# Kernel tuning notes

Measured on AMD Instinct MI355X. Metric: run time of the kernel, lower is better.

## Reference

```python
import jax, jax.numpy as jnp
import numpy as np

N_MEL = 80
NEG = -1e30  # log-zero sentinel, as in the torch module


def setup_inputs() -> dict:
    key = jax.random.key(0)
    k1, k2, k3, k4 = jax.random.split(key, 4)
    B, txt_T, mel_T = 16, 128, 512
    mu_logvar = jax.random.normal(k1, (B, txt_T, 2 * N_MEL), dtype=jnp.float32)
    melspec = jax.random.normal(k2, (B, N_MEL, mel_T), dtype=jnp.float32)
    text_lengths = jax.random.randint(k3, (B,), txt_T // 2, txt_T + 1, dtype=jnp.int32)
    mel_lengths = jax.random.randint(k4, (B,), mel_T // 2, mel_T + 1, dtype=jnp.int32)
    return dict(mu_logvar=mu_logvar, melspec=melspec,
                text_lengths=text_lengths, mel_lengths=mel_lengths)


def _log_prob_matrix(mu_logvar, melspec):
    # mu_logvar: [B, txt_T, 2*n_mel]; melspec: [B, n_mel, mel_T]
    mu = mu_logvar[:, :, :N_MEL]            # [B, txt_T, n_mel]
    logvar = mu_logvar[:, :, N_MEL:]        # [B, txt_T, n_mel]
    x = jnp.transpose(melspec, (0, 2, 1))   # [B, mel_T, n_mel]
    diff = x[:, None, :, :] - mu[:, :, None, :]          # [B, txt_T, mel_T, n_mel]
    quad = diff * diff * jnp.exp(-logvar)[:, :, None, :] + logvar[:, :, None, :]
    return -0.5 * jnp.mean(quad, axis=3)    # [B, txt_T, mel_T]


def _log_alpha_last(log_prob_matrix, text_lengths, mel_lengths):
    B, txt_T, mel_T = log_prob_matrix.shape
    # init: log_alpha[:, :, 0] = NEG except [:,0,0] = logp[:,0,0]
    init = jnp.full((B, txt_T), NEG, log_prob_matrix.dtype).at[:, 0].set(log_prob_matrix[:, 0, 0])
    logp_t = jnp.moveaxis(log_prob_matrix, 2, 0)  # [mel_T, B, txt_T]

    def step(prev, lp):
        # shift-by-one along text axis (monotonic alignment: stay or advance)
        shifted = jnp.concatenate([jnp.full((B, 1), NEG, prev.dtype), prev[:, :-1]], axis=1)
        cur = jnp.logaddexp(prev + 1e-30, shifted + 1e-30) + lp
        return cur, cur

    _, rest = jax.lax.scan(step, init, logp_t[1:])
    log_alpha = jnp.concatenate([init[None], rest], axis=0)  # [mel_T, B, txt_T]
    b = jnp.arange(B)
    return log_alpha[mel_lengths - 1, b, text_lengths - 1]   # [B]


def reference(mu_logvar, melspec, text_lengths, mel_lengths):
    log_prob_matrix = _log_prob_matrix(mu_logvar, melspec)
    alpha_last = _log_alpha_last(log_prob_matrix, text_lengths, mel_lengths)
    alpha_last = alpha_last / mel_lengths
    mdn_loss = -jnp.mean(alpha_last)
    return (mdn_loss, log_prob_matrix)
```

## Files before the change

kernel.cpp:

```cpp
#include <hip/hip_runtime.h>

#define NEG  (-1e30f)
#define LN2F 0.69314718056f

#define B_   16
#define TXT_ 128
#define MEL_ 512
#define NM_  80
#define IT_  8

typedef float vf2 __attribute__((ext_vector_type(2)));

__global__ __launch_bounds__(512) void lp_kernel(
    const float* __restrict__ mu_logvar,
    const float* __restrict__ melspec,
    float* __restrict__ lp_out,
    float* __restrict__ wT,
    float* __restrict__ out0)
{
    const int i0 = blockIdx.x * IT_;
    const int b  = blockIdx.y;
    const int t  = threadIdx.x;

    __shared__ float2 s_wb[IT_][NM_];
    __shared__ float  s_cp[IT_ * NM_];
    __shared__ float  s_cc[IT_];

    for (int u = t; u < IT_ * NM_; u += 512) {
        int ii = u / NM_;
        int n  = u - ii * NM_;
        const float* row = mu_logvar + (size_t)(b * TXT_ + i0 + ii) * (2 * NM_);
        float mu = row[n];
        float lv = row[NM_ + n];
        float w  = __expf(-lv);
        s_wb[ii][n] = make_float2(w, -2.f * mu * w);
        s_cp[u]     = mu * mu * w + lv;
    }
    __syncthreads();
    if (t < IT_) {
        float c = 0.f;
        #pragma unroll
        for (int n = 0; n < NM_; ++n) c += s_cp[t * NM_ + n];
        s_cc[t] = c;
    }
    __syncthreads();

    const float* xcol = melspec + (size_t)b * NM_ * MEL_ + t;
    float acc[IT_];
    #pragma unroll
    for (int ii = 0; ii < IT_; ++ii) acc[ii] = 0.f;

    #pragma unroll 4
    for (int n = 0; n < NM_; ++n) {
        float x  = xcol[(size_t)n * MEL_];
        float x2 = x * x;
        #pragma unroll
        for (int ii = 0; ii < IT_; ++ii) {
            float2 wb = s_wb[ii][n];
            acc[ii] = fmaf(wb.x, x2, fmaf(wb.y, x, acc[ii]));
        }
    }

    const size_t rowbase = ((size_t)(b * TXT_ + i0)) * MEL_ + t;
    #pragma unroll
    for (int ii = 0; ii < IT_; ++ii) {
        lp_out[rowbase + (size_t)ii * MEL_] =
            (-0.5f / (float)NM_) * (acc[ii] + s_cc[ii]);
    }

    if (i0 == 0 && t == 0) wT[(size_t)b * MEL_ * TXT_] = 0.f;
    if (i0 == 0 && b == 0 && t == 0) *out0 = 0.f;
}

__global__ __launch_bounds__(256) void wt_kernel(
    const float* __restrict__ lp,
    const int* __restrict__ mel_len,
    float* __restrict__ wT)
{
    __shared__ float tileT[32][TXT_ + 1];
    __shared__ float pmax[32][8];
    __shared__ float psum[32];

    const int t0  = blockIdx.x * 32;
    const int b   = blockIdx.y;
    const int tid = threadIdx.x;

    const float* src = lp + (size_t)b * TXT_ * MEL_ + t0;
    for (int u = tid; u < TXT_ * 32; u += 256) {
        int i = u >> 5, c = u & 31;
        tileT[c][i] = src[(size_t)i * MEL_ + c];
    }
    __syncthreads();

    {
        int tt = tid >> 3, g = tid & 7;
        float m = NEG;
        #pragma unroll
        for (int k = 0; k < 16; ++k) m = fmaxf(m, tileT[tt][g * 16 + k]);
        pmax[tt][g] = m;
    }
    __syncthreads();
    if (tid < 32) {
        float m = pmax[tid][0];
        #pragma unroll
        for (int g = 1; g < 8; ++g) m = fmaxf(m, pmax[tid][g]);
        pmax[tid][0] = m;
        int tg = t0 + tid;
        int TendM1 = mel_len[b] - 1;
        psum[tid] = (tg >= 1 && tg <= TendM1) ? (m + LN2F) : 0.f;
    }
    __syncthreads();

    float* dstb = wT + (size_t)b * MEL_ * TXT_;
    for (int u = tid; u < 32 * TXT_; u += 256) {
        int tt = u >> 7, i = u & 127;
        int tg = t0 + tt;
        if (tg != 0)
            dstb[(size_t)tg * TXT_ + i] =
                __expf(tileT[tt][i] - pmax[tt][0] - LN2F);
    }

    if (tid == 0) {
        float s = 0.f;
        #pragma unroll
        for (int k = 0; k < 32; ++k) s += psum[k];
        if (t0 == 0) s += tileT[0][0];
        atomicAdd(&dstb[0], s);
    }
}

__device__ __forceinline__ float dpp_shr1_zero(float x) {
    int r = __builtin_amdgcn_update_dpp(
        0, __builtin_bit_cast(int, x), 0x138 , 0xf, 0xf, false);
    return __builtin_bit_cast(float, r);
}

#define DPPMAX(M, CTRL, RM)                                               \
    do {                                                                  \
        int _t = __builtin_amdgcn_update_dpp(                             \
            __builtin_bit_cast(int, M), __builtin_bit_cast(int, M),       \
            CTRL, RM, 0xf, false);                                        \
        M = fmaxf(M, __builtin_bit_cast(float, _t));                      \
    } while (0)

#define GLOAD2(DST, PTR) \
    asm volatile("global_load_dwordx2 %0, %1, off" : "=v"(DST) : "v"(PTR))
#define VWAIT12(A,B,C,D2) \
    asm volatile("s_waitcnt vmcnt(12)" : "+v"(A), "+v"(B), "+v"(C), "+v"(D2))

__global__ __launch_bounds__(64) void scan_kernel(
    const float* __restrict__ wT,
    const int* __restrict__ text_len, const int* __restrict__ mel_len,
    float* __restrict__ out0)
{
    const int b = blockIdx.x;
    const int l = threadIdx.x;
    const float* base = wT + (size_t)b * MEL_ * TXT_;
    const float* wb_  = base + 2 * l;
    const int Tend = mel_len[b], TendM1 = Tend - 1;

    float s0 = (l == 0) ? 1.f : 0.f;
    float s1 = 0.f;
    float fin0 = 0.f, fin1 = 0.f;
    int   shift_acc = 0, fsh = 0;
    int   t_cur = 1;
    int   t_pf  = 17;

    vf2 q0,q1,q2,q3,q4,q5,q6,q7,q8,q9,q10,q11,q12,q13,q14,q15;
    {
        const float* p;
        #define INIT(Q, ROW) p = wb_ + (size_t)(ROW) * TXT_; GLOAD2(Q, p)
        INIT(q0,1);  INIT(q1,2);  INIT(q2,3);   INIT(q3,4);
        INIT(q4,5);  INIT(q5,6);  INIT(q6,7);   INIT(q7,8);
        INIT(q8,9);  INIT(q9,10); INIT(q10,11); INIT(q11,12);
        INIT(q12,13); INIT(q13,14); INIT(q14,15); INIT(q15,16);
        #undef INIT
    }

    #define STEP(Q)                                          \
        do {                                                 \
            float nb  = dpp_shr1_zero(s1);                   \
            float ns0 = (s0 + nb) * (Q).x;                   \
            float ns1 = (s1 + s0) * (Q).y;                   \
            bool hit = (t_cur == TendM1);                    \
            fin0 = hit ? ns0 : fin0;                         \
            fin1 = hit ? ns1 : fin1;                         \
            fsh  = hit ? shift_acc : fsh;                    \
            s0 = ns0; s1 = ns1; ++t_cur;                     \
        } while (0)

    #define REFILL(Q)                                        \
        do {                                                 \
            int rr = min(t_pf, MEL_ - 1);                    \
            const float* p_ = wb_ + (size_t)rr * TXT_;       \
            GLOAD2(Q, p_);                                   \
            ++t_pf;                                          \
        } while (0)

    #define GROUP(QA,QB,QC,QD)                               \
        do {                                                 \
            VWAIT12(QA,QB,QC,QD);                            \
            STEP(QA); STEP(QB); STEP(QC); STEP(QD);          \
            REFILL(QA); REFILL(QB); REFILL(QC); REFILL(QD);  \
        } while (0)

    for (int t0 = 1; t0 <= TendM1; t0 += 16) {
        GROUP(q0,q1,q2,q3);
        GROUP(q4,q5,q6,q7);
        GROUP(q8,q9,q10,q11);
        GROUP(q12,q13,q14,q15);

        float mm = fmaxf(s0, s1);
        DPPMAX(mm, 0x111, 0xf);
        DPPMAX(mm, 0x112, 0xf);
        DPPMAX(mm, 0x114, 0xf);
        DPPMAX(mm, 0x118, 0xf);
        DPPMAX(mm, 0x142, 0xa);
        DPPMAX(mm, 0x143, 0xc);
        float M = __builtin_bit_cast(
            float, __builtin_amdgcn_readlane(__builtin_bit_cast(int, mm), 63));
        if (M > 0.f) {
            int e;
            (void)frexpf(M, &e);
            float sc = ldexpf(1.f, -e);
            s0 *= sc; s1 *= sc;
            shift_acc += e;
        }
    }
    #undef STEP
    #undef REFILL
    #undef GROUP

    int jstar = text_len[b] - 1;
    float vs = (jstar & 1) ? fin1 : fin0;
    int   vh = fsh;
    vs = __shfl(vs, jstar >> 1);
    vh = __shfl(vh, jstar >> 1);
    if (l == 0) {
        float musum = base[0];
        float val   = __logf(vs) + (float)vh * LN2F + musum;
        atomicAdd(out0, -(val / (float)Tend) * (1.f / (float)B_));
    }
}

extern "C" void kernel_launch(void* const* d_in, const int* in_sizes, int n_in,
                              void* d_out, int out_size, void* d_ws, size_t ws_size,
                              hipStream_t stream) {
    const float* mu_logvar = (const float*)d_in[0];
    const float* melspec   = (const float*)d_in[1];
    const int*   text_len  = (const int*)d_in[2];
    const int*   mel_len   = (const int*)d_in[3];

    float* out    = (float*)d_out;
    float* lp_out = out + 1;
    float* wT     = (float*)d_ws;

    dim3 g1(TXT_ / IT_, B_);
    lp_kernel<<<g1, MEL_, 0, stream>>>(mu_logvar, melspec, lp_out, wT, out);
    dim3 g2(MEL_ / 32, B_);
    wt_kernel<<<g2, 256, 0, stream>>>(lp_out, mel_len, wT);
    scan_kernel<<<B_, 64, 0, stream>>>(wT, text_len, mel_len, out);
}
```

Before: 102.3 us.

## Pack two time steps per lane into dwordx4 loads for the scan kernel

The weight tensor written by wt_kernel is repacked so that each lane's two text positions for two consecutive time steps sit contiguously, letting scan_kernel issue one 16-byte load per two steps instead of one 8-byte load per step. Prefetch depth in time steps doubles with the same 16 registers, and renormalisation moves from every 16 steps to every 16 steps inside a 32-step loop. The per-batch sum is moved out of the weight buffer into a separate stash. The latency-bound serial scan should stall less on memory. The cost is scattered stores in wt_kernel and a possible over-read past mel_len at the tail.

```diff
diff --git a/kernel.cpp b/kernel.cpp
--- a/kernel.cpp
+++ b/kernel.cpp
@@ -8,14 +8,15 @@
 #define MEL_ 512
 #define NM_  80
 #define IT_  8
-
-typedef float vf2 __attribute__((ext_vector_type(2)));
+#define PKB_ (MEL_ * TXT_)
+
+typedef float vf4 __attribute__((ext_vector_type(4)));
 
 __global__ __launch_bounds__(512) void lp_kernel(
     const float* __restrict__ mu_logvar,
     const float* __restrict__ melspec,
     float* __restrict__ lp_out,
-    float* __restrict__ wT,
+    float* __restrict__ stash,
     float* __restrict__ out0)
 {
     const int i0 = blockIdx.x * IT_;
@@ -68,14 +69,15 @@
             (-0.5f / (float)NM_) * (acc[ii] + s_cc[ii]);
     }
 
-    if (i0 == 0 && t == 0) wT[(size_t)b * MEL_ * TXT_] = 0.f;
+    if (i0 == 0 && t == 0) stash[b] = 0.f;
     if (i0 == 0 && b == 0 && t == 0) *out0 = 0.f;
 }
 
 __global__ __launch_bounds__(256) void wt_kernel(
     const float* __restrict__ lp,
     const int* __restrict__ mel_len,
-    float* __restrict__ wT)
+    float* __restrict__ wpk,
+    float* __restrict__ stash)
 {
     __shared__ float tileT[32][TXT_ + 1];
     __shared__ float pmax[32][8];
@@ -111,13 +113,16 @@
     }
     __syncthreads();
 
-    float* dstb = wT + (size_t)b * MEL_ * TXT_;
+    float* dstb = wpk + (size_t)b * PKB_;
     for (int u = tid; u < 32 * TXT_; u += 256) {
         int tt = u >> 7, i = u & 127;
         int tg = t0 + tt;
-        if (tg != 0)
-            dstb[(size_t)tg * TXT_ + i] =
-                __expf(tileT[tt][i] - pmax[tt][0] - LN2F);
+        if (tg >= 1) {
+            int tm = tg - 1;
+            size_t off = (size_t)(tm >> 1) * 256 + (i >> 1) * 4
+                       + (tm & 1) * 2 + (i & 1);
+            dstb[off] = __expf(tileT[tt][i] - pmax[tt][0] - LN2F);
+        }
     }
 
     if (tid == 0) {
@@ -125,7 +130,7 @@
         #pragma unroll
         for (int k = 0; k < 32; ++k) s += psum[k];
         if (t0 == 0) s += tileT[0][0];
-        atomicAdd(&dstb[0], s);
+        atomicAdd(&stash[b], s);
     }
 }
 
@@ -143,20 +148,20 @@
         M = fmaxf(M, __builtin_bit_cast(float, _t));                      \
     } while (0)
 
-#define GLOAD2(DST, PTR) \
-    asm volatile("global_load_dwordx2 %0, %1, off" : "=v"(DST) : "v"(PTR))
+#define GLOAD4(DST, PTR) \
+    asm volatile("global_load_dwordx4 %0, %1, off" : "=v"(DST) : "v"(PTR))
 #define VWAIT12(A,B,C,D2) \
     asm volatile("s_waitcnt vmcnt(12)" : "+v"(A), "+v"(B), "+v"(C), "+v"(D2))
 
 __global__ __launch_bounds__(64) void scan_kernel(
-    const float* __restrict__ wT,
+    const float* __restrict__ wpk,
+    const float* __restrict__ stash,
     const int* __restrict__ text_len, const int* __restrict__ mel_len,
     float* __restrict__ out0)
 {
     const int b = blockIdx.x;
     const int l = threadIdx.x;
-    const float* base = wT + (size_t)b * MEL_ * TXT_;
-    const float* wb_  = base + 2 * l;
+    const float* wb_ = wpk + (size_t)b * PKB_ + 4 * l;
     const int Tend = mel_len[b], TendM1 = Tend - 1;
 
     float s0 = (l == 0) ? 1.f : 0.f;
@@ -164,72 +169,88 @@
     float fin0 = 0.f, fin1 = 0.f;
     int   shift_acc = 0, fsh = 0;
     int   t_cur = 1;
-    int   t_pf  = 17;
-
-    vf2 q0,q1,q2,q3,q4,q5,q6,q7,q8,q9,q10,q11,q12,q13,q14,q15;
+    int   p_pf  = 16;
+
+    vf4 q0,q1,q2,q3,q4,q5,q6,q7,q8,q9,q10,q11,q12,q13,q14,q15;
     {
-        const float* p;
-        #define INIT(Q, ROW) p = wb_ + (size_t)(ROW) * TXT_; GLOAD2(Q, p)
-        INIT(q0,1);  INIT(q1,2);  INIT(q2,3);   INIT(q3,4);
-        INIT(q4,5);  INIT(q5,6);  INIT(q6,7);   INIT(q7,8);
-        INIT(q8,9);  INIT(q9,10); INIT(q10,11); INIT(q11,12);
-        INIT(q12,13); INIT(q13,14); INIT(q14,15); INIT(q15,16);
-        #undef INIT
-    }
-
-    #define STEP(Q)                                          \
+        const float* pp;
+        #define INITQ(Q, P) pp = wb_ + (size_t)(P) * 256; GLOAD4(Q, pp)
+        INITQ(q0,0);   INITQ(q1,1);   INITQ(q2,2);   INITQ(q3,3);
+        INITQ(q4,4);   INITQ(q5,5);   INITQ(q6,6);   INITQ(q7,7);
+        INITQ(q8,8);   INITQ(q9,9);   INITQ(q10,10); INITQ(q11,11);
+        INITQ(q12,12); INITQ(q13,13); INITQ(q14,14); INITQ(q15,15);
+        #undef INITQ
+    }
+
+    #define CSTEP2(Q)                                        \
         do {                                                 \
-            float nb  = dpp_shr1_zero(s1);                   \
-            float ns0 = (s0 + nb) * (Q).x;                   \
-            float ns1 = (s1 + s0) * (Q).y;                   \
-            bool hit = (t_cur == TendM1);                    \
-            fin0 = hit ? ns0 : fin0;                         \
-            fin1 = hit ? ns1 : fin1;                         \
-            fsh  = hit ? shift_acc : fsh;                    \
-            s0 = ns0; s1 = ns1; ++t_cur;                     \
+            {                                                \
+                float nb  = dpp_shr1_zero(s1);               \
+                float ns0 = (s0 + nb) * (Q).x;               \
+                float ns1 = (s1 + s0) * (Q).y;               \
+                bool hit = (t_cur == TendM1);                \
+                fin0 = hit ? ns0 : fin0;                     \
+                fin1 = hit ? ns1 : fin1;                     \
+                fsh  = hit ? shift_acc : fsh;                \
+                s0 = ns0; s1 = ns1; ++t_cur;                 \
+            }                                                \
+            {                                                \
+                float nb  = dpp_shr1_zero(s1);               \
+                float ns0 = (s0 + nb) * (Q).z;               \
+                float ns1 = (s1 + s0) * (Q).w;               \
+                bool hit = (t_cur == TendM1);                \
+                fin0 = hit ? ns0 : fin0;                     \
+                fin1 = hit ? ns1 : fin1;                     \
+                fsh  = hit ? shift_acc : fsh;                \
+                s0 = ns0; s1 = ns1; ++t_cur;                 \
+            }                                                \
         } while (0)
 
     #define REFILL(Q)                                        \
         do {                                                 \
-            int rr = min(t_pf, MEL_ - 1);                    \
-            const float* p_ = wb_ + (size_t)rr * TXT_;       \
-            GLOAD2(Q, p_);                                   \
-            ++t_pf;                                          \
+            int rr = min(p_pf, 255);                         \
+            const float* p_ = wb_ + (size_t)rr * 256;        \
+            GLOAD4(Q, p_);                                   \
+            ++p_pf;                                          \
         } while (0)
 
     #define GROUP(QA,QB,QC,QD)                               \
         do {                                                 \
             VWAIT12(QA,QB,QC,QD);                            \
-            STEP(QA); STEP(QB); STEP(QC); STEP(QD);          \
+            CSTEP2(QA); CSTEP2(QB); CSTEP2(QC); CSTEP2(QD);  \
             REFILL(QA); REFILL(QB); REFILL(QC); REFILL(QD);  \
         } while (0)
 
-    for (int t0 = 1; t0 <= TendM1; t0 += 16) {
-        GROUP(q0,q1,q2,q3);
-        GROUP(q4,q5,q6,q7);
-        GROUP(q8,q9,q10,q11);
-        GROUP(q12,q13,q14,q15);
-
-        float mm = fmaxf(s0, s1);
-        DPPMAX(mm, 0x111, 0xf);
-        DPPMAX(mm, 0x112, 0xf);
-        DPPMAX(mm, 0x114, 0xf);
-        DPPMAX(mm, 0x118, 0xf);
-        DPPMAX(mm, 0x142, 0xa);
-        DPPMAX(mm, 0x143, 0xc);
-        float M = __builtin_bit_cast(
-            float, __builtin_amdgcn_readlane(__builtin_bit_cast(int, mm), 63));
-        if (M > 0.f) {
-            int e;
-            (void)frexpf(M, &e);
-            float sc = ldexpf(1.f, -e);
-            s0 *= sc; s1 *= sc;
-            shift_acc += e;
-        }
-    }
-    #undef STEP
+    #define RENORM                                                            \
+        do {                                                                  \
+            float mm = fmaxf(s0, s1);                                         \
+            DPPMAX(mm, 0x111, 0xf);                            \
+            DPPMAX(mm, 0x112, 0xf);                            \
+            DPPMAX(mm, 0x114, 0xf);                            \
+            DPPMAX(mm, 0x118, 0xf);                            \
+            DPPMAX(mm, 0x142, 0xa);             \
+            DPPMAX(mm, 0x143, 0xc);             \
+            float M = __builtin_bit_cast(float,                               \
+                __builtin_amdgcn_readlane(__builtin_bit_cast(int, mm), 63));  \
+            if (M > 0.f) {                                                    \
+                int e;                                                        \
+                (void)frexpf(M, &e);                                          \
+                float sc = ldexpf(1.f, -e);                                   \
+                s0 *= sc; s1 *= sc;                                           \
+                shift_acc += e;                                               \
+            }                                                                 \
+        } while (0)
+
+    for (int t0 = 1; t0 <= TendM1; t0 += 32) {
+        GROUP(q0,q1,q2,q3);   GROUP(q4,q5,q6,q7);
+        RENORM;
+        GROUP(q8,q9,q10,q11); GROUP(q12,q13,q14,q15);
+        RENORM;
+    }
+    #undef CSTEP2
     #undef REFILL
     #undef GROUP
+    #undef RENORM
 
     int jstar = text_len[b] - 1;
     float vs = (jstar & 1) ? fin1 : fin0;
@@ -237,7 +258,7 @@
     vs = __shfl(vs, jstar >> 1);
     vh = __shfl(vh, jstar >> 1);
     if (l == 0) {
-        float musum = base[0];
+        float musum = stash[b];
         float val   = __logf(vs) + (float)vh * LN2F + musum;
         atomicAdd(out0, -(val / (float)Tend) * (1.f / (float)B_));
     }
@@ -253,11 +274,12 @@
 
     float* out    = (float*)d_out;
     float* lp_out = out + 1;
-    float* wT     = (float*)d_ws;
+    float* wpk    = (float*)d_ws;
+    float* stash  = (float*)d_ws + (size_t)B_ * PKB_;
 
     dim3 g1(TXT_ / IT_, B_);
-    lp_kernel<<<g1, MEL_, 0, stream>>>(mu_logvar, melspec, lp_out, wT, out);
+    lp_kernel<<<g1, MEL_, 0, stream>>>(mu_logvar, melspec, lp_out, stash, out);
     dim3 g2(MEL_ / 32, B_);
-    wt_kernel<<<g2, 256, 0, stream>>>(lp_out, mel_len, wT);
-    scan_kernel<<<B_, 64, 0, stream>>>(wT, text_len, mel_len, out);
-}
+    wt_kernel<<<g2, 256, 0, stream>>>(lp_out, mel_len, wpk, stash);
+    scan_kernel<<<B_, 64, 0, stream>>>(wpk, stash, text_len, mel_len, out);
+}
```

Result: no change. 102.9 us (+0.6%).
